# Optimization experiments

Measured on AMD Instinct MI355X. Metric: run time of the kernel, lower is better.

The kernel has to match this reference:

```python
import jax, jax.numpy as jnp
import numpy as np

NEG_SLOPE = 0.01
LN_EPS = 1e-5

def _layer_norm(h, g, b):
    mu = jnp.mean(h, axis=-1, keepdims=True)
    var = jnp.mean(jnp.square(h - mu), axis=-1, keepdims=True)
    return (h - mu) * jax.lax.rsqrt(var + LN_EPS) * g + b

def _mlp(h, Wa, ba, g, be, Wb, bb):
    h = h @ Wa + ba
    h = jnp.where(h >= 0, h, NEG_SLOPE * h)  # LeakyReLU
    h = _layer_norm(h, g, be)
    return h @ Wb + bb

def setup_inputs() -> dict:
    N, E = 50000, 800000
    DN, DE, DG, DO = 128, 64, 32, 128
    key = jax.random.key(0)
    ks = jax.random.split(key, 16)
    def lin(k, fan_in, fan_out):
        lim = 1.0 / np.sqrt(fan_in)
        k1, k2 = jax.random.split(k)
        W = jax.random.uniform(k1, (fan_in, fan_out), jnp.float32, -lim, lim)
        b = jax.random.uniform(k2, (fan_out,), jnp.float32, -lim, lim)
        return W, b
    W1a, b1a = lin(ks[0], DN + DE + DG, DO)
    W1b, b1b = lin(ks[1], DO, DO)
    W2a, b2a = lin(ks[2], DN + DO, DO)
    W2b, b2b = lin(ks[3], DO, DO)
    return {
        "x": jax.random.normal(ks[4], (N, DN), jnp.float32),
        "edge_index": jax.random.randint(ks[5], (2, E), 0, N, jnp.int32),
        "edge_attr": jax.random.normal(ks[6], (E, DE), jnp.float32),
        "u": jax.random.normal(ks[7], (DG,), jnp.float32),
        "batch": jnp.zeros((N,), jnp.int32),
        "W1a": W1a, "b1a": b1a,
        "g1": jnp.ones((DO,), jnp.float32), "be1": jnp.zeros((DO,), jnp.float32),
        "W1b": W1b, "b1b": b1b,
        "W2a": W2a, "b2a": b2a,
        "g2": jnp.ones((DO,), jnp.float32), "be2": jnp.zeros((DO,), jnp.float32),
        "W2b": W2b, "b2b": b2b,
    }

def reference(x, edge_index, edge_attr, u, batch,
              W1a, b1a, g1, be1, W1b, b1b,
              W2a, b2a, g2, be2, W2b, b2b):
    src, dest = edge_index[0], edge_index[1]
    E = edge_attr.shape[0]
    N = x.shape[0]
    # gather + concat: [E, DN+DE+DG]
    h = jnp.concatenate([x[src], edge_attr,
                         jnp.broadcast_to(u[None, :], (E, u.shape[0]))], axis=1)
    h = _mlp(h, W1a, b1a, g1, be1, W1b, b1b)
    # scatter_mean by dest
    sums = jax.ops.segment_sum(h, dest, num_segments=N)
    cnt = jax.ops.segment_sum(jnp.ones((E,), h.dtype), dest, num_segments=N)
    agg = sums / jnp.maximum(cnt, 1.0)[:, None]
    return _mlp(jnp.concatenate([x, agg], axis=1), W2a, b2a, g2, be2, W2b, b2b)
```

## Files before the change

kernel.cpp:

```cpp
#include <hip/hip_runtime.h>
#include <hip/hip_fp16.h>
#include <hip/hip_bf16.h>

constexpr int DN = 128, DE = 64, DG = 32, DO = 128;
constexpr int K1 = DN + DE + DG;
constexpr int K2 = DN + DO;
constexpr float NEG_SLOPE = 0.01f;
constexpr float LN_EPS = 1e-5f;

constexpr int EPB = 128;
constexpr int NB  = 64;
constexpr int A_LD = 40;
constexpr int B_LD = 40;
constexpr int H_LD = 264;

typedef __attribute__((ext_vector_type(8))) short bf16x8;
typedef __attribute__((ext_vector_type(4))) float f32x4;

__device__ inline unsigned short f2bf(float f) {
    unsigned u = __builtin_bit_cast(unsigned, f);
    u += 0x7FFFu + ((u >> 16) & 1u);
    return (unsigned short)(u >> 16);
}

__global__ __launch_bounds__(256) void edge_kernel(
    const float* __restrict__ x, const int* __restrict__ edge_index,
    const float* __restrict__ edge_attr, const float* __restrict__ u,
    const float* __restrict__ W1a,
    const float* __restrict__ b1a, const float* __restrict__ g1,
    const float* __restrict__ be1,
    __half* __restrict__ sums, float* __restrict__ cnt, int E)
{
    __shared__ unsigned short s_a[EPB * A_LD];
    __shared__ unsigned short s_b[128 * B_LD];
    __shared__ int s_src[EPB], s_dst[EPB];

    const int tid  = threadIdx.x;
    const int lane = tid & 63, wave = tid >> 6;
    const int l15  = lane & 15, quad = lane >> 4;
    const int ebase  = blockIdx.x * EPB;
    const int evalid = min(EPB, E - ebase);

    if (tid < EPB) {
        int e = ebase + tid;
        bool v = tid < evalid;
        s_src[tid] = v ? edge_index[e] : 0;
        s_dst[tid] = v ? edge_index[E + e] : 0;
    }
    __syncthreads();

    f32x4 acc[2][8];
#pragma unroll
    for (int mt = 0; mt < 2; ++mt)
#pragma unroll
        for (int nt = 0; nt < 8; ++nt) acc[mt][nt] = (f32x4){0.f, 0.f, 0.f, 0.f};

    const int e0 = tid >> 3;
    const int k4 = (tid & 7) * 4;

    for (int ks = 0; ks < 7; ++ks) {
        const int kbase = ks * 32;
#pragma unroll
        for (int it = 0; it < 4; ++it) {
            int e = e0 + it * 32;
            float4 v;
            if (ks < 4) {
                v = *(const float4*)&x[(long)s_src[e] * DN + kbase + k4];
            } else if (ks < 6) {
                long row = min((long)(ebase + e), (long)E - 1);
                v = *(const float4*)&edge_attr[row * DE + (kbase - DN) + k4];
            } else {
                v = *(const float4*)&u[k4];
            }
            ushort4 b;
            b.x = f2bf(v.x); b.y = f2bf(v.y); b.z = f2bf(v.z); b.w = f2bf(v.w);
            *(ushort4*)&s_a[e * A_LD + k4] = b;
        }
#pragma unroll
        for (int it = 0; it < 8; ++it) {
            int p = tid + it * 256;
            int k2 = p >> 7, n = p & 127;
            float w0 = W1a[(long)(kbase + 2 * k2) * DO + n];
            float w1 = W1a[(long)(kbase + 2 * k2 + 1) * DO + n];
            unsigned pk = (unsigned)f2bf(w0) | ((unsigned)f2bf(w1) << 16);
            *(unsigned*)&s_b[n * B_LD + 2 * k2] = pk;
        }
        __syncthreads();
        bf16x8 a0 = *(const bf16x8*)&s_a[(wave * 32 + l15) * A_LD + quad * 8];
        bf16x8 a1 = *(const bf16x8*)&s_a[(wave * 32 + 16 + l15) * A_LD + quad * 8];
#pragma unroll
        for (int nt = 0; nt < 8; ++nt) {
            bf16x8 b = *(const bf16x8*)&s_b[(nt * 16 + l15) * B_LD + quad * 8];
            acc[0][nt] = __builtin_amdgcn_mfma_f32_16x16x32_bf16(a0, b, acc[0][nt], 0, 0, 0);
            acc[1][nt] = __builtin_amdgcn_mfma_f32_16x16x32_bf16(a1, b, acc[1][nt], 0, 0, 0);
        }
        __syncthreads();
    }

    float ba[8], gg[8], bb[8];
#pragma unroll
    for (int nt = 0; nt < 8; ++nt) {
        int col = nt * 16 + l15;
        ba[nt] = b1a[col]; gg[nt] = g1[col]; bb[nt] = be1[col];
    }
#pragma unroll
    for (int mt = 0; mt < 2; ++mt) {
#pragma unroll
        for (int r = 0; r < 4; ++r) {
            float v[8];
            float s = 0.f, q = 0.f;
#pragma unroll
            for (int nt = 0; nt < 8; ++nt) {
                float t = acc[mt][nt][r] + ba[nt];
                t = (t >= 0.f) ? t : NEG_SLOPE * t;
                v[nt] = t; s += t; q += t * t;
            }
#pragma unroll
            for (int off = 1; off < 16; off <<= 1) {
                s += __shfl_xor(s, off, 64);
                q += __shfl_xor(q, off, 64);
            }
            float mu  = s * (1.f / DO);
            float var = q * (1.f / DO) - mu * mu;
            float rs  = rsqrtf(var + LN_EPS);
            int lrow = wave * 32 + mt * 16 + quad * 4 + r;
            bool doat = (lrow < evalid);
            long base = (long)s_dst[lrow] * DO;
#pragma unroll
            for (int nt = 0; nt < 8; ++nt) {
                float h  = (v[nt] - mu) * rs * gg[nt] + bb[nt];
                float hp = __shfl_xor(h, 1, 64);
                if (doat && ((l15 & 1) == 0)) {
                    __half2 pv = __halves2half2(__float2half_rn(h),
                                                __float2half_rn(hp));
                    unsafeAtomicAdd((__half2*)&sums[base + nt * 16 + l15], pv);
                }
            }
        }
    }
    if (tid < evalid) atomicAdd(&cnt[s_dst[tid]], 1.0f);
}

__global__ __launch_bounds__(256) void node_kernel(
    const float* __restrict__ x, const __half* __restrict__ sums,
    const float* __restrict__ cnt,
    const float* __restrict__ W1b, const float* __restrict__ b1b,
    const float* __restrict__ W2a, const float* __restrict__ b2a,
    const float* __restrict__ g2, const float* __restrict__ be2,
    const float* __restrict__ W2b, const float* __restrict__ b2b,
    float* __restrict__ out, int N)
{
    __shared__ unsigned short s_h[NB * H_LD];
    __shared__ unsigned short s_b[128 * B_LD];
    __shared__ float s_cf[NB];

    const int tid  = threadIdx.x;
    const int lane = tid & 63, wave = tid >> 6;
    const int l15  = lane & 15, quad = lane >> 4;
    const int nbase  = blockIdx.x * NB;
    const int nvalid = min(NB, N - nbase);

#pragma unroll
    for (int i = 0; i < 8; ++i) {
        int p = tid + i * 256;
        int row = p >> 5, c4 = (p & 31) * 4;
        int node = nbase + min(row, nvalid - 1);
        float4 v = *(const float4*)&x[(long)node * DN + c4];
        ushort4 b;
        b.x = f2bf(v.x); b.y = f2bf(v.y); b.z = f2bf(v.z); b.w = f2bf(v.w);
        *(ushort4*)&s_h[row * H_LD + c4] = b;
    }
#pragma unroll
    for (int i = 0; i < 8; ++i) {
        int p = tid + i * 256;
        int row = p >> 5, c = (p & 31) * 4;
        int node = nbase + min(row, nvalid - 1);
        float cn = cnt[node];
        if (c == 0) s_cf[row] = (cn > 0.f) ? 1.f : 0.f;
        float inv = 1.f / fmaxf(cn, 1.f);
        const __half2* sp = (const __half2*)&sums[(long)node * DO + c];
        float2 a0 = __half22float2(sp[0]);
        float2 a1 = __half22float2(sp[1]);
        ushort4 b;
        b.x = f2bf(a0.x * inv); b.y = f2bf(a0.y * inv);
        b.z = f2bf(a1.x * inv); b.w = f2bf(a1.y * inv);
        *(ushort4*)&s_h[row * H_LD + DN + c] = b;
    }

    const unsigned short* aPtr = &s_h[(wave * 16 + l15) * H_LD];

    f32x4 acc[8];

#pragma unroll
    for (int nt = 0; nt < 8; ++nt) acc[nt] = (f32x4){0.f, 0.f, 0.f, 0.f};
    for (int ks = 0; ks < 4; ++ks) {
        __syncthreads();
#pragma unroll
        for (int it = 0; it < 8; ++it) {
            int p = tid + it * 256;
            int k2 = p >> 7, n = p & 127;
            float w0 = W1b[(long)(ks * 32 + 2 * k2) * DO + n];
            float w1 = W1b[(long)(ks * 32 + 2 * k2 + 1) * DO + n];
            unsigned pk = (unsigned)f2bf(w0) | ((unsigned)f2bf(w1) << 16);
            *(unsigned*)&s_b[n * B_LD + 2 * k2] = pk;
        }
        __syncthreads();
        bf16x8 a = *(const bf16x8*)&aPtr[DN + ks * 32 + quad * 8];
#pragma unroll
        for (int nt = 0; nt < 8; ++nt) {
            bf16x8 b = *(const bf16x8*)&s_b[(nt * 16 + l15) * B_LD + quad * 8];
            acc[nt] = __builtin_amdgcn_mfma_f32_16x16x32_bf16(a, b, acc[nt], 0, 0, 0);
        }
    }
    __syncthreads();
    {
        float b1v[8];
#pragma unroll
        for (int nt = 0; nt < 8; ++nt) b1v[nt] = b1b[nt * 16 + l15];
#pragma unroll
        for (int reg = 0; reg < 4; ++reg) {
            int row = wave * 16 + quad * 4 + reg;
            float cf = s_cf[row];
#pragma unroll
            for (int nt = 0; nt < 8; ++nt) {
                float v = acc[nt][reg] + cf * b1v[nt];
                s_h[row * H_LD + DN + nt * 16 + l15] = f2bf(v);
            }
        }
    }

#pragma unroll
    for (int nt = 0; nt < 8; ++nt) acc[nt] = (f32x4){0.f, 0.f, 0.f, 0.f};
    for (int ks = 0; ks < 8; ++ks) {
        __syncthreads();
#pragma unroll
        for (int it = 0; it < 8; ++it) {
            int p = tid + it * 256;
            int k2 = p >> 7, n = p & 127;
            float w0 = W2a[(long)(ks * 32 + 2 * k2) * DO + n];
            float w1 = W2a[(long)(ks * 32 + 2 * k2 + 1) * DO + n];
            unsigned pk = (unsigned)f2bf(w0) | ((unsigned)f2bf(w1) << 16);
            *(unsigned*)&s_b[n * B_LD + 2 * k2] = pk;
        }
        __syncthreads();
        bf16x8 a = *(const bf16x8*)&aPtr[ks * 32 + quad * 8];
#pragma unroll
        for (int nt = 0; nt < 8; ++nt) {
            bf16x8 b = *(const bf16x8*)&s_b[(nt * 16 + l15) * B_LD + quad * 8];
            acc[nt] = __builtin_amdgcn_mfma_f32_16x16x32_bf16(a, b, acc[nt], 0, 0, 0);
        }
    }
    __syncthreads();
    {
        float ba[8], gg[8], bb[8];
#pragma unroll
        for (int nt = 0; nt < 8; ++nt) {
            int col = nt * 16 + l15;
            ba[nt] = b2a[col]; gg[nt] = g2[col]; bb[nt] = be2[col];
        }
#pragma unroll
        for (int reg = 0; reg < 4; ++reg) {
            float v[8];
            float s = 0.f, q = 0.f;
#pragma unroll
            for (int nt = 0; nt < 8; ++nt) {
                float t = acc[nt][reg] + ba[nt];
                t = (t >= 0.f) ? t : NEG_SLOPE * t;
                v[nt] = t; s += t; q += t * t;
            }
#pragma unroll
            for (int off = 1; off < 16; off <<= 1) {
                s += __shfl_xor(s, off, 64);
                q += __shfl_xor(q, off, 64);
            }
            float mu  = s * (1.f / DO);
            float var = q * (1.f / DO) - mu * mu;
            float rs  = rsqrtf(var + LN_EPS);
            int row = wave * 16 + quad * 4 + reg;
#pragma unroll
            for (int nt = 0; nt < 8; ++nt) {
                float h = (v[nt] - mu) * rs * gg[nt] + bb[nt];
                s_h[row * H_LD + nt * 16 + l15] = f2bf(h);
            }
        }
    }

#pragma unroll
    for (int nt = 0; nt < 8; ++nt) acc[nt] = (f32x4){0.f, 0.f, 0.f, 0.f};
    for (int ks = 0; ks < 4; ++ks) {
        __syncthreads();
#pragma unroll
        for (int it = 0; it < 8; ++it) {
            int p = tid + it * 256;
            int k2 = p >> 7, n = p & 127;
            float w0 = W2b[(long)(ks * 32 + 2 * k2) * DO + n];
            float w1 = W2b[(long)(ks * 32 + 2 * k2 + 1) * DO + n];
            unsigned pk = (unsigned)f2bf(w0) | ((unsigned)f2bf(w1) << 16);
            *(unsigned*)&s_b[n * B_LD + 2 * k2] = pk;
        }
        __syncthreads();
        bf16x8 a = *(const bf16x8*)&aPtr[ks * 32 + quad * 8];
#pragma unroll
        for (int nt = 0; nt < 8; ++nt) {
            bf16x8 b = *(const bf16x8*)&s_b[(nt * 16 + l15) * B_LD + quad * 8];
            acc[nt] = __builtin_amdgcn_mfma_f32_16x16x32_bf16(a, b, acc[nt], 0, 0, 0);
        }
    }
    {
        float b2v[8];
#pragma unroll
        for (int nt = 0; nt < 8; ++nt) b2v[nt] = b2b[nt * 16 + l15];
#pragma unroll
        for (int reg = 0; reg < 4; ++reg) {
            int row = wave * 16 + quad * 4 + reg;
            if (row < nvalid) {
                long base = (long)(nbase + row) * DO;
#pragma unroll
                for (int nt = 0; nt < 8; ++nt)
                    out[base + nt * 16 + l15] = acc[nt][reg] + b2v[nt];
            }
        }
    }
}

extern "C" void kernel_launch(void* const* d_in, const int* in_sizes, int n_in,
                              void* d_out, int out_size, void* d_ws, size_t ws_size,
                              hipStream_t stream)
{
    const float* x          = (const float*)d_in[0];
    const int*   edge_index = (const int*)d_in[1];
    const float* edge_attr  = (const float*)d_in[2];
    const float* u          = (const float*)d_in[3];
    const float* W1a = (const float*)d_in[5];
    const float* b1a = (const float*)d_in[6];
    const float* g1  = (const float*)d_in[7];
    const float* be1 = (const float*)d_in[8];
    const float* W1b = (const float*)d_in[9];
    const float* b1b = (const float*)d_in[10];
    const float* W2a = (const float*)d_in[11];
    const float* b2a = (const float*)d_in[12];
    const float* g2  = (const float*)d_in[13];
    const float* be2 = (const float*)d_in[14];
    const float* W2b = (const float*)d_in[15];
    const float* b2b = (const float*)d_in[16];

    const int N = in_sizes[0] / DN;
    const int E = in_sizes[2] / DE;
    float* out  = (float*)d_out;

    __half* sums = (__half*)d_ws;
    float*  cnt  = (float*)(sums + (size_t)N * DO);

    (void)hipMemsetAsync(d_ws, 0,
                         (size_t)N * DO * sizeof(__half) + (size_t)N * sizeof(float),
                         stream);

    const int eblocks = (E + EPB - 1) / EPB;
    edge_kernel<<<eblocks, 256, 0, stream>>>(
        x, edge_index, edge_attr, u, W1a, b1a, g1, be1, sums, cnt, E);

    const int nblocks = (N + NB - 1) / NB;
    node_kernel<<<nblocks, 256, 0, stream>>>(
        x, sums, cnt, W1b, b1b, W2a, b2a, g2, be2, W2b, b2b, out, N);
}
```

Before: 740.8 us.

## Pre-pack bf16 weights in MFMA fragment order and load operands directly into registers

Adds a small prep kernel that converts all four weight matrices to bf16 once per call, storing them in the exact per-lane MFMA B-fragment layout in workspace. The edge and node kernels then read A fragments straight from global memory into registers and B fragments from the packed table. This removes the shared-memory staging, the repeated per-block fp32-to-bf16 weight conversion and the block-wide barriers. The node kernel keeps only a per-wave shared buffer for intermediate activations. The trade-off is an extra launch and more scattered global loads per lane in place of coalesced cooperative tile loads.

Measured after the change: 711.5 us. 4.0% less time.

```diff
diff --git a/kernel.cpp b/kernel.cpp
--- a/kernel.cpp
+++ b/kernel.cpp
@@ -4,15 +4,12 @@
 
 constexpr int DN = 128, DE = 64, DG = 32, DO = 128;
 constexpr int K1 = DN + DE + DG;
-constexpr int K2 = DN + DO;
 constexpr float NEG_SLOPE = 0.01f;
 constexpr float LN_EPS = 1e-5f;
 
 constexpr int EPB = 128;
 constexpr int NB  = 64;
-constexpr int A_LD = 40;
-constexpr int B_LD = 40;
-constexpr int H_LD = 264;
+constexpr int T_LD = 136;
 
 typedef __attribute__((ext_vector_type(8))) short bf16x8;
 typedef __attribute__((ext_vector_type(4))) float f32x4;
@@ -23,78 +20,102 @@
     return (unsigned short)(u >> 16);
 }
 
+__device__ inline bf16x8 pk8(float4 p, float4 q) {
+    bf16x8 r;
+    r[0] = (short)f2bf(p.x); r[1] = (short)f2bf(p.y);
+    r[2] = (short)f2bf(p.z); r[3] = (short)f2bf(p.w);
+    r[4] = (short)f2bf(q.x); r[5] = (short)f2bf(q.y);
+    r[6] = (short)f2bf(q.z); r[7] = (short)f2bf(q.w);
+    return r;
+}
+
+__global__ void wprep_kernel(const float* __restrict__ W1a,
+                             const float* __restrict__ W1b,
+                             const float* __restrict__ W2a,
+                             const float* __restrict__ W2b,
+                             unsigned short* __restrict__ tab) {
+    int idx = blockIdx.x * 256 + threadIdx.x;
+    if (idx >= 23 * 512) return;
+    int slabset = idx >> 9;
+    int rem = idx & 511;
+    const float* W; int sl;
+    if (slabset < 7)       { W = W1a; sl = slabset; }
+    else if (slabset < 11) { W = W1b; sl = slabset - 7; }
+    else if (slabset < 19) { W = W2a; sl = slabset - 11; }
+    else                   { W = W2b; sl = slabset - 19; }
+    int nt = rem >> 6, lane = rem & 63;
+    int quad = lane >> 4, l15 = lane & 15;
+    int n = nt * 16 + l15;
+    int k0 = sl * 32 + quad * 8;
+    union { ushort4 u4[2]; unsigned short s[8]; } o;
+#pragma unroll
+    for (int j = 0; j < 8; ++j) o.s[j] = f2bf(W[(long)(k0 + j) * DO + n]);
+    *(ushort4*)&tab[(long)idx * 8]     = o.u4[0];
+    *(ushort4*)&tab[(long)idx * 8 + 4] = o.u4[1];
+}
+
 __global__ __launch_bounds__(256) void edge_kernel(
     const float* __restrict__ x, const int* __restrict__ edge_index,
     const float* __restrict__ edge_attr, const float* __restrict__ u,
-    const float* __restrict__ W1a,
+    const unsigned short* __restrict__ tab,
     const float* __restrict__ b1a, const float* __restrict__ g1,
     const float* __restrict__ be1,
     __half* __restrict__ sums, float* __restrict__ cnt, int E)
 {
-    __shared__ unsigned short s_a[EPB * A_LD];
-    __shared__ unsigned short s_b[128 * B_LD];
     __shared__ int s_src[EPB], s_dst[EPB];
 
-    const int tid  = threadIdx.x;
-    const int lane = tid & 63, wave = tid >> 6;
-    const int l15  = lane & 15, quad = lane >> 4;
-    const int ebase  = blockIdx.x * EPB;
+    const int tid = threadIdx.x, lane = tid & 63, wave = tid >> 6;
+    const int l15 = lane & 15, quad = lane >> 4;
+    const int ebase = blockIdx.x * EPB;
     const int evalid = min(EPB, E - ebase);
 
     if (tid < EPB) {
-        int e = ebase + tid;
-        bool v = tid < evalid;
+        int e = ebase + tid; bool v = tid < evalid;
         s_src[tid] = v ? edge_index[e] : 0;
         s_dst[tid] = v ? edge_index[E + e] : 0;
     }
     __syncthreads();
 
+    const int r0 = wave * 32 + l15, r1 = r0 + 16;
+    const long xs0 = (long)s_src[r0] * DN;
+    const long xs1 = (long)s_src[r1] * DN;
+    const long er0 = (long)min(ebase + r0, E - 1) * DE;
+    const long er1 = (long)min(ebase + r1, E - 1) * DE;
+    const bf16x8* tW1a = (const bf16x8*)tab;
+    const int kq = quad * 8;
+
     f32x4 acc[2][8];
 #pragma unroll
     for (int mt = 0; mt < 2; ++mt)
 #pragma unroll
         for (int nt = 0; nt < 8; ++nt) acc[mt][nt] = (f32x4){0.f, 0.f, 0.f, 0.f};
 
-    const int e0 = tid >> 3;
-    const int k4 = (tid & 7) * 4;
-
+#pragma unroll
     for (int ks = 0; ks < 7; ++ks) {
-        const int kbase = ks * 32;
-#pragma unroll
-        for (int it = 0; it < 4; ++it) {
-            int e = e0 + it * 32;
-            float4 v;
-            if (ks < 4) {
-                v = *(const float4*)&x[(long)s_src[e] * DN + kbase + k4];
-            } else if (ks < 6) {
-                long row = min((long)(ebase + e), (long)E - 1);
-                v = *(const float4*)&edge_attr[row * DE + (kbase - DN) + k4];
-            } else {
-                v = *(const float4*)&u[k4];
-            }
-            ushort4 b;
-            b.x = f2bf(v.x); b.y = f2bf(v.y); b.z = f2bf(v.z); b.w = f2bf(v.w);
-            *(ushort4*)&s_a[e * A_LD + k4] = b;
-        }
-#pragma unroll
-        for (int it = 0; it < 8; ++it) {
-            int p = tid + it * 256;
-            int k2 = p >> 7, n = p & 127;
-            float w0 = W1a[(long)(kbase + 2 * k2) * DO + n];
-            float w1 = W1a[(long)(kbase + 2 * k2 + 1) * DO + n];
-            unsigned pk = (unsigned)f2bf(w0) | ((unsigned)f2bf(w1) << 16);
-            *(unsigned*)&s_b[n * B_LD + 2 * k2] = pk;
-        }
-        __syncthreads();
-        bf16x8 a0 = *(const bf16x8*)&s_a[(wave * 32 + l15) * A_LD + quad * 8];
-        bf16x8 a1 = *(const bf16x8*)&s_a[(wave * 32 + 16 + l15) * A_LD + quad * 8];
-#pragma unroll
-        for (int nt = 0; nt < 8; ++nt) {
-            bf16x8 b = *(const bf16x8*)&s_b[(nt * 16 + l15) * B_LD + quad * 8];
+        float4 p0, q0, p1, q1;
+        if (ks < 4) {
+            const float* b0 = &x[xs0 + ks * 32 + kq];
+            const float* b1 = &x[xs1 + ks * 32 + kq];
+            p0 = *(const float4*)b0; q0 = *(const float4*)(b0 + 4);
+            p1 = *(const float4*)b1; q1 = *(const float4*)(b1 + 4);
+        } else if (ks < 6) {
+            int c = ks * 32 - DN + kq;
+            const float* b0 = &edge_attr[er0 + c];
+            const float* b1 = &edge_attr[er1 + c];
+            p0 = *(const float4*)b0; q0 = *(const float4*)(b0 + 4);
+            p1 = *(const float4*)b1; q1 = *(const float4*)(b1 + 4);
+        } else {
+            p0 = *(const float4*)&u[kq]; q0 = *(const float4*)&u[kq + 4];
+            p1 = p0; q1 = q0;
+        }
+        bf16x8 a0 = pk8(p0, q0);
+        bf16x8 a1 = pk8(p1, q1);
+#pragma unroll
+        for (int nt = 0; nt < 8; ++nt) {
+            bf16x8 b = tW1a[(ks * 8 + nt) * 64 + lane];
             acc[0][nt] = __builtin_amdgcn_mfma_f32_16x16x32_bf16(a0, b, acc[0][nt], 0, 0, 0);
             acc[1][nt] = __builtin_amdgcn_mfma_f32_16x16x32_bf16(a1, b, acc[1][nt], 0, 0, 0);
         }
-        __syncthreads();
     }
 
     float ba[8], gg[8], bb[8];
@@ -143,114 +164,77 @@
 
 __global__ __launch_bounds__(256) void node_kernel(
     const float* __restrict__ x, const __half* __restrict__ sums,
-    const float* __restrict__ cnt,
-    const float* __restrict__ W1b, const float* __restrict__ b1b,
-    const float* __restrict__ W2a, const float* __restrict__ b2a,
+    const float* __restrict__ cnt, const unsigned short* __restrict__ tab,
+    const float* __restrict__ b1b, const float* __restrict__ b2a,
     const float* __restrict__ g2, const float* __restrict__ be2,
-    const float* __restrict__ W2b, const float* __restrict__ b2b,
+    const float* __restrict__ b2b,
     float* __restrict__ out, int N)
 {
-    __shared__ unsigned short s_h[NB * H_LD];
-    __shared__ unsigned short s_b[128 * B_LD];
-    __shared__ float s_cf[NB];
-
-    const int tid  = threadIdx.x;
-    const int lane = tid & 63, wave = tid >> 6;
-    const int l15  = lane & 15, quad = lane >> 4;
-    const int nbase  = blockIdx.x * NB;
-    const int nvalid = min(NB, N - nbase);
-
-#pragma unroll
-    for (int i = 0; i < 8; ++i) {
-        int p = tid + i * 256;
-        int row = p >> 5, c4 = (p & 31) * 4;
-        int node = nbase + min(row, nvalid - 1);
-        float4 v = *(const float4*)&x[(long)node * DN + c4];
-        ushort4 b;
-        b.x = f2bf(v.x); b.y = f2bf(v.y); b.z = f2bf(v.z); b.w = f2bf(v.w);
-        *(ushort4*)&s_h[row * H_LD + c4] = b;
-    }
-#pragma unroll
-    for (int i = 0; i < 8; ++i) {
-        int p = tid + i * 256;
-        int row = p >> 5, c = (p & 31) * 4;
-        int node = nbase + min(row, nvalid - 1);
-        float cn = cnt[node];
-        if (c == 0) s_cf[row] = (cn > 0.f) ? 1.f : 0.f;
-        float inv = 1.f / fmaxf(cn, 1.f);
-        const __half2* sp = (const __half2*)&sums[(long)node * DO + c];
-        float2 a0 = __half22float2(sp[0]);
-        float2 a1 = __half22float2(sp[1]);
-        ushort4 b;
-        b.x = f2bf(a0.x * inv); b.y = f2bf(a0.y * inv);
-        b.z = f2bf(a1.x * inv); b.w = f2bf(a1.y * inv);
-        *(ushort4*)&s_h[row * H_LD + DN + c] = b;
-    }
-
-    const unsigned short* aPtr = &s_h[(wave * 16 + l15) * H_LD];
+    __shared__ unsigned short s_t[4][16 * T_LD];
+
+    const int tid = threadIdx.x, lane = tid & 63, wave = tid >> 6;
+    const int l15 = lane & 15, quad = lane >> 4;
+    const int nbase = blockIdx.x * NB;
+
+    const bf16x8* tW1b = (const bf16x8*)tab + 7 * 512;
+    const bf16x8* tW2a = (const bf16x8*)tab + 11 * 512;
+    const bf16x8* tW2b = (const bf16x8*)tab + 19 * 512;
+
+    const int nodeA = min(nbase + wave * 16 + l15, N - 1);
+    const float invc = 1.f / fmaxf(cnt[nodeA], 1.f);
+    const int kq = quad * 8;
 
     f32x4 acc[8];
 
 #pragma unroll
     for (int nt = 0; nt < 8; ++nt) acc[nt] = (f32x4){0.f, 0.f, 0.f, 0.f};
+#pragma unroll
     for (int ks = 0; ks < 4; ++ks) {
-        __syncthreads();
-#pragma unroll
-        for (int it = 0; it < 8; ++it) {
-            int p = tid + it * 256;
-            int k2 = p >> 7, n = p & 127;
-            float w0 = W1b[(long)(ks * 32 + 2 * k2) * DO + n];
-            float w1 = W1b[(long)(ks * 32 + 2 * k2 + 1) * DO + n];
-            unsigned pk = (unsigned)f2bf(w0) | ((unsigned)f2bf(w1) << 16);
-            *(unsigned*)&s_b[n * B_LD + 2 * k2] = pk;
-        }
-        __syncthreads();
-        bf16x8 a = *(const bf16x8*)&aPtr[DN + ks * 32 + quad * 8];
-#pragma unroll
-        for (int nt = 0; nt < 8; ++nt) {
-            bf16x8 b = *(const bf16x8*)&s_b[(nt * 16 + l15) * B_LD + quad * 8];
+        const __half2* sp = (const __half2*)(sums + (long)nodeA * DO + ks * 32 + kq);
+        float2 f0 = __half22float2(sp[0]);
+        float2 f1 = __half22float2(sp[1]);
+        float2 f2 = __half22float2(sp[2]);
+        float2 f3 = __half22float2(sp[3]);
+        float4 p = {f0.x * invc, f0.y * invc, f1.x * invc, f1.y * invc};
+        float4 q = {f2.x * invc, f2.y * invc, f3.x * invc, f3.y * invc};
+        bf16x8 a = pk8(p, q);
+#pragma unroll
+        for (int nt = 0; nt < 8; ++nt) {
+            bf16x8 b = tW1b[(ks * 8 + nt) * 64 + lane];
             acc[nt] = __builtin_amdgcn_mfma_f32_16x16x32_bf16(a, b, acc[nt], 0, 0, 0);
         }
     }
-    __syncthreads();
     {
-        float b1v[8];
-#pragma unroll
-        for (int nt = 0; nt < 8; ++nt) b1v[nt] = b1b[nt * 16 + l15];
 #pragma unroll
         for (int reg = 0; reg < 4; ++reg) {
-            int row = wave * 16 + quad * 4 + reg;
-            float cf = s_cf[row];
-#pragma unroll
-            for (int nt = 0; nt < 8; ++nt) {
-                float v = acc[nt][reg] + cf * b1v[nt];
-                s_h[row * H_LD + DN + nt * 16 + l15] = f2bf(v);
+            int lrow = quad * 4 + reg;
+            int nodeC = nbase + wave * 16 + lrow;
+            float cf = (nodeC < N && cnt[min(nodeC, N - 1)] > 0.f) ? 1.f : 0.f;
+#pragma unroll
+            for (int nt = 0; nt < 8; ++nt) {
+                float v = acc[nt][reg] + cf * b1b[nt * 16 + l15];
+                s_t[wave][lrow * T_LD + nt * 16 + l15] = f2bf(v);
             }
         }
     }
 
 #pragma unroll
     for (int nt = 0; nt < 8; ++nt) acc[nt] = (f32x4){0.f, 0.f, 0.f, 0.f};
+#pragma unroll
     for (int ks = 0; ks < 8; ++ks) {
-        __syncthreads();
-#pragma unroll
-        for (int it = 0; it < 8; ++it) {
-            int p = tid + it * 256;
-            int k2 = p >> 7, n = p & 127;
-            float w0 = W2a[(long)(ks * 32 + 2 * k2) * DO + n];
-            float w1 = W2a[(long)(ks * 32 + 2 * k2 + 1) * DO + n];
-            unsigned pk = (unsigned)f2bf(w0) | ((unsigned)f2bf(w1) << 16);
-            *(unsigned*)&s_b[n * B_LD + 2 * k2] = pk;
-        }
-        __syncthreads();
-        bf16x8 a = *(const bf16x8*)&aPtr[ks * 32 + quad * 8];
-#pragma unroll
-        for (int nt = 0; nt < 8; ++nt) {
-            bf16x8 b = *(const bf16x8*)&s_b[(nt * 16 + l15) * B_LD + quad * 8];
+        bf16x8 a;
+        if (ks < 4) {
+            const float* b0 = &x[(long)nodeA * DN + ks * 32 + kq];
+            a = pk8(*(const float4*)b0, *(const float4*)(b0 + 4));
+        } else {
+            a = *(const bf16x8*)&s_t[wave][l15 * T_LD + (ks - 4) * 32 + kq];
+        }
+#pragma unroll
+        for (int nt = 0; nt < 8; ++nt) {
+            bf16x8 b = tW2a[(ks * 8 + nt) * 64 + lane];
             acc[nt] = __builtin_amdgcn_mfma_f32_16x16x32_bf16(a, b, acc[nt], 0, 0, 0);
         }
     }
-    __syncthreads();
     {
         float ba[8], gg[8], bb[8];
 #pragma unroll
@@ -276,48 +260,35 @@
             float mu  = s * (1.f / DO);
             float var = q * (1.f / DO) - mu * mu;
             float rs  = rsqrtf(var + LN_EPS);
-            int row = wave * 16 + quad * 4 + reg;
+            int lrow = quad * 4 + reg;
 #pragma unroll
             for (int nt = 0; nt < 8; ++nt) {
                 float h = (v[nt] - mu) * rs * gg[nt] + bb[nt];
-                s_h[row * H_LD + nt * 16 + l15] = f2bf(h);
+                s_t[wave][lrow * T_LD + nt * 16 + l15] = f2bf(h);
             }
         }
     }
 
 #pragma unroll
     for (int nt = 0; nt < 8; ++nt) acc[nt] = (f32x4){0.f, 0.f, 0.f, 0.f};
+#pragma unroll
     for (int ks = 0; ks < 4; ++ks) {
-        __syncthreads();
-#pragma unroll
-        for (int it = 0; it < 8; ++it) {
-            int p = tid + it * 256;
-            int k2 = p >> 7, n = p & 127;
-            float w0 = W2b[(long)(ks * 32 + 2 * k2) * DO + n];
-            float w1 = W2b[(long)(ks * 32 + 2 * k2 + 1) * DO + n];
-            unsigned pk = (unsigned)f2bf(w0) | ((unsigned)f2bf(w1) << 16);
-            *(unsigned*)&s_b[n * B_LD + 2 * k2] = pk;
-        }
-        __syncthreads();
-        bf16x8 a = *(const bf16x8*)&aPtr[ks * 32 + quad * 8];
-#pragma unroll
-        for (int nt = 0; nt < 8; ++nt) {
-            bf16x8 b = *(const bf16x8*)&s_b[(nt * 16 + l15) * B_LD + quad * 8];
+        bf16x8 a = *(const bf16x8*)&s_t[wave][l15 * T_LD + ks * 32 + kq];
+#pragma unroll
+        for (int nt = 0; nt < 8; ++nt) {
+            bf16x8 b = tW2b[(ks * 8 + nt) * 64 + lane];
             acc[nt] = __builtin_amdgcn_mfma_f32_16x16x32_bf16(a, b, acc[nt], 0, 0, 0);
         }
     }
     {
-        float b2v[8];
-#pragma unroll
-        for (int nt = 0; nt < 8; ++nt) b2v[nt] = b2b[nt * 16 + l15];
 #pragma unroll
         for (int reg = 0; reg < 4; ++reg) {
-            int row = wave * 16 + quad * 4 + reg;
-            if (row < nvalid) {
-                long base = (long)(nbase + row) * DO;
+            int nodeC = nbase + wave * 16 + quad * 4 + reg;
+            if (nodeC < N) {
+                long base = (long)nodeC * DO;
 #pragma unroll
                 for (int nt = 0; nt < 8; ++nt)
-                    out[base + nt * 16 + l15] = acc[nt][reg] + b2v[nt];
+                    out[base + nt * 16 + l15] = acc[nt][reg] + b2b[nt * 16 + l15];
             }
         }
     }
@@ -350,16 +321,21 @@
 
     __half* sums = (__half*)d_ws;
     float*  cnt  = (float*)(sums + (size_t)N * DO);
+    size_t tab_off = (size_t)N * DO * sizeof(__half) + (size_t)N * sizeof(float);
+    tab_off = (tab_off + 15) & ~(size_t)15;
+    unsigned short* tab = (unsigned short*)((char*)d_ws + tab_off);
 
     (void)hipMemsetAsync(d_ws, 0,
                          (size_t)N * DO * sizeof(__half) + (size_t)N * sizeof(float),
                          stream);
 
+    wprep_kernel<<<(23 * 512 + 255) / 256, 256, 0, stream>>>(W1a, W1b, W2a, W2b, tab);
+
     const int eblocks = (E + EPB - 1) / EPB;
     edge_kernel<<<eblocks, 256, 0, stream>>>(
-        x, edge_index, edge_attr, u, W1a, b1a, g1, be1, sums, cnt, E);
+        x, edge_index, edge_attr, u, tab, b1a, g1, be1, sums, cnt, E);
 
     const int nblocks = (N + NB - 1) / NB;
     node_kernel<<<nblocks, 256, 0, stream>>>(
-        x, sums, cnt, W1b, b1b, W2a, b2a, g2, be2, W2b, b2b, out, N);
-}
+        x, sums, cnt, tab, b1b, b2a, g2, be2, b2b, out, N);
+}
```
